# Performance work log

Hardware: AMD Instinct MI355X
Metric: run time of the kernel (lower is better)

Reference implementation:

```python
import jax, jax.numpy as jnp
import numpy as np

N = 2048          # num agents / graph nodes
D = 128           # n_actor == n_map
ALPHA = 0.2       # GAT leakyrelu alpha
NEG = -1e9
X_IDX = [4, 9, 14, 19]   # actors_inter_cat time indices per LSTM step
E_IDX = [0, 4, 9, 14]    # graph_adjs time indices per LSTM step


def setup_inputs() -> dict:
    key = jax.random.key(0)
    ks = jax.random.split(key, 10)
    xavier = lambda k, shape: jax.random.uniform(
        k, shape, jnp.float32, -1.0, 1.0) * 1.414 * np.sqrt(6.0 / (shape[-2] + shape[-1]))
    actors_inter_cat = jax.random.normal(ks[0], (N, 20, D), jnp.float32)
    graph_adjs = jax.random.randint(ks[1], (N, 20, N), 0, 2, jnp.int32)
    # 4 GAT_SRF gates (forget, input, input_cell, output), stacked on leading axis
    Wg = xavier(ks[2], (4, 2 * D, D))          # gate projection W: in=2*D, out=D
    ag = xavier(ks[3], (4, 2 * D))             # attention vector a (2*out_features,)
    W = xavier(ks[4], (D, D))                  # GAT cell output projection
    b = xavier(ks[5], (1, D))
    h0 = xavier(ks[6], (1, D))
    conv_w = jax.random.normal(ks[7], (3, D, D, 2), jnp.float32) * (1.0 / np.sqrt(2 * D))
    conv_b = jax.random.normal(ks[8], (3, D), jnp.float32) * 0.01
    return {"actors_inter_cat": actors_inter_cat, "graph_adjs": graph_adjs,
            "Wg": Wg, "ag": ag, "W": W, "b": b, "h0": h0,
            "conv_w": conv_w, "conv_b": conv_b}


def _gat_gates(gin, mask, Wg, ag):
    # gin: (N, 2D); mask: (N, N) bool. Computes all 4 GAT_SRF gates at once.
    Wh = jnp.einsum('nf,gfo->gno', gin, Wg)                 # (4, N, D)
    s_src = jnp.einsum('gno,go->gn', Wh, ag[:, :D])         # a^T [Wh_i ..]
    s_dst = jnp.einsum('gno,go->gn', Wh, ag[:, D:])
    e = jax.nn.leaky_relu(s_src[:, :, None] + s_dst[:, None, :], ALPHA)  # (4,N,N)
    e = jnp.where(mask[None], e, NEG)
    attn = jax.nn.softmax(e, axis=-1)
    return jax.nn.elu(jnp.einsum('gnm,gmo->gno', attn, Wh))  # concat=True -> ELU


def reference(actors_inter_cat, graph_adjs, Wg, ag, W, b, h0, conv_w, conv_b):
    n = actors_inter_cat.shape[0]
    cell = actors_inter_cat[:, 0, :]
    hidden = jnp.broadcast_to(h0, (n, D))
    outs = []
    for t in range(4):  # fixed 4-step recurrence
        X = actors_inter_cat[:, X_IDX[t], :]
        mask = graph_adjs[:, E_IDX[t], :] > 0
        gin = jnp.concatenate([X, hidden], axis=1)          # (N, 2D)
        g = _gat_gates(gin, mask, Wg, ag)                   # (4, N, D)
        forget = jax.nn.sigmoid(g[0])
        inp_gate = jax.nn.sigmoid(g[1])
        inp_cell = jnp.tanh(g[2])
        out_gate = jax.nn.sigmoid(g[3])
        cell = cell * forget + inp_gate * inp_cell
        hidden = jnp.tanh(cell) * out_gate
        outs.append(jax.nn.sigmoid(hidden @ W + b))
    y = jnp.stack(outs, axis=2)                             # (N, D, 4)
    for l in range(3):  # kernel-2 Conv1d stack: length 4 -> 3 -> 2 -> 1
        y = (jnp.einsum('nct,oc->not', y[:, :, :-1], conv_w[l, :, :, 0])
             + jnp.einsum('nct,oc->not', y[:, :, 1:], conv_w[l, :, :, 1])
             + conv_b[l][None, :, None])
    return y[:, :, 0]                                       # squeeze -> (N, D)
```

## Files before the change

kernel.cpp:

```cpp
#include <hip/hip_runtime.h>

typedef __attribute__((ext_vector_type(8))) short short8;
typedef __attribute__((ext_vector_type(4))) float floatx4;

#define MFMA16(a,b,c) __builtin_amdgcn_mfma_f32_16x16x32_bf16(a,b,c,0,0,0)

__device__ __forceinline__ unsigned short f2bf(float f){
  unsigned u = __float_as_uint(f);
  u += 0x7fffu + ((u >> 16) & 1u);
  return (unsigned short)(u >> 16);
}
__device__ __forceinline__ float sigm(float x){ return 1.f/(1.f+__expf(-x)); }


__global__ __launch_bounds__(256) void prep_kernel(const float* __restrict__ actors,
    const float* __restrict__ Wg, const float* __restrict__ cw, const int* __restrict__ adj,
    float* __restrict__ cell, unsigned short* __restrict__ WgA, float* __restrict__ cwT,
    unsigned long long* __restrict__ bm){
  int bid = blockIdx.x;
  if (bid < 1024){
    int idx = bid*256 + threadIdx.x;
    int n = idx >> 7, c = idx & 127;
    cell[idx] = actors[(size_t)n*2560 + c];
  } else if (bid < 1536){
    int e = (bid-1024)*256 + threadIdx.x;
    int g = e >> 15, o = (e >> 8) & 127, k = e & 255;
    unsigned short v = f2bf(Wg[(size_t)g*32768 + k*128 + o]);
    int off = ((o>>4)*8 + (k>>5))*512 + (((k>>3)&3)*16 + (o&15))*8 + (k&7);
    WgA[(size_t)g*32768 + off] = v;
  } else if (bid < 1728){
    int e = (bid-1536)*256 + threadIdx.x;
    int l = e >> 14, rr = e & 16383, k = rr >> 7, o = rr & 127;
    cwT[(size_t)l*32768 + k*256 + o]       = cw[(size_t)l*32768 + o*256 + k*2];
    cwT[(size_t)l*32768 + k*256 + 128 + o] = cw[(size_t)l*32768 + o*256 + k*2 + 1];
  } else {
    const int E[4] = {0,4,9,14};
    int mb = bid - 1728;
    int t = mb & 3, nblk = mb >> 2;
    int wv = threadIdx.x >> 6, lane = threadIdx.x & 63;
    int n = nblk*4 + wv;
    const int* row = adj + (size_t)n*40960 + (size_t)E[t]*2048;
    unsigned long long* outp = bm + ((size_t)t*2048 + n)*32;
    for (int it=0; it<32; ++it){
      unsigned long long bal = __ballot(row[it*64 + lane] > 0);
      if (lane == 0) outp[it] = bal;
    }
  }
}

__global__ __launch_bounds__(1024) void gatewh_kernel(const float* __restrict__ actors,
    const float* __restrict__ gbuf, float* __restrict__ cell, const float* __restrict__ h0,
    const float* __restrict__ W, const float* __restrict__ bvec,
    const unsigned short* __restrict__ WgA, const float* __restrict__ ag,
    float* __restrict__ y, unsigned short* __restrict__ WhB,
    float* __restrict__ spart, int xoff, int t){
  __shared__ float hl[16][132];
  __shared__ __align__(16) unsigned short ginb[16*264];
  __shared__ float sredS[4][4][16], sredD[4][4][16];
  int bx = blockIdx.x;
  int tile = bx >> 1, ohalf = bx & 1;
  int n0 = tile*16, tid = threadIdx.x;
  int row = tid>>6, q = tid&63;
  {
    int o0 = q*2;
    if (t == 0){
      *(float2*)&hl[row][o0] = *(const float2*)(h0 + o0);
    } else {
      size_t idx = (size_t)(n0+row)*128 + o0;
      float2 ga = *(const float2*)(gbuf+idx);
      float2 gb = *(const float2*)(gbuf+262144+idx);
      float2 gc = *(const float2*)(gbuf+524288+idx);
      float2 gd = *(const float2*)(gbuf+786432+idx);
      float2 cv = *(const float2*)(cell+idx);
      float fg[2]={ga.x,ga.y}, ig[2]={gb.x,gb.y};
      float ic[2]={gc.x,gc.y}, og[2]={gd.x,gd.y};
      float cc[2]={cv.x,cv.y};
      float clv[2];
      #pragma unroll
      for (int j=0;j<2;++j){
        clv[j] = cc[j]*sigm(fg[j]) + sigm(ig[j])*tanhf(ic[j]);
        hl[row][o0+j] = tanhf(clv[j])*sigm(og[j]);
      }
      if (ohalf == 0)
        *(float2*)(cell+idx) = (float2){clv[0],clv[1]};
    }
  }
  __syncthreads();
  if (t >= 1){
    int oc = ohalf*64 + q;
    float a0 = bvec[oc];
    const float* hr = hl[row];
    for (int k=0;k<128;++k)
      a0 += hr[k] * W[(size_t)k*128 + oc];
    y[(size_t)(t-1)*262144 + (size_t)(n0+row)*128 + oc] = sigm(a0);
  }
  if (q < 16){
    const float* ap = actors + (size_t)(n0+row)*2560 + xoff + q*8;
    float4 a = *(const float4*)ap, bb = *(const float4*)(ap+4);
    unsigned short tmp[8] = {f2bf(a.x),f2bf(a.y),f2bf(a.z),f2bf(a.w),
                             f2bf(bb.x),f2bf(bb.y),f2bf(bb.z),f2bf(bb.w)};
    *(uint4*)&ginb[row*264 + q*8] = *(const uint4*)tmp;
  } else if (q < 32){
    int c0 = (q-16)*8;
    unsigned short tmp[8];
    #pragma unroll
    for (int j=0;j<8;++j) tmp[j] = f2bf(hl[row][c0+j]);
    *(uint4*)&ginb[row*264 + 128 + c0] = *(const uint4*)tmp;
  }
  __syncthreads();
  int w = tid>>6, lane = tid&63, quad = lane>>4, l16 = lane&15;
  int m32 = tile>>1, min32 = (tile&1)*16 + l16;
  int qp = min32>>3, jp = min32&7;
  {
    int cidx = w;
    int g = cidx>>2, o16q = cidx&3, o16 = ohalf*4 + o16q;
    floatx4 acc = {0.f,0.f,0.f,0.f};
    const unsigned short* wa = WgA + (size_t)g*32768;
    #pragma unroll
    for (int kh=0; kh<8; ++kh){
      short8 bfr = *(const short8*)&ginb[l16*264 + kh*32 + quad*8];
      short8 a0 = *(const short8*)(wa + (size_t)((o16*8 + kh)*64 + lane)*8);
      acc = MFMA16(a0, bfr, acc);
    }
    float ps = 0.f, pd = 0.f;
    unsigned short* wb = WhB + (size_t)(g*8 + o16)*32768 + m32*512 + qp*128 + jp;
    const float* agp = ag + g*256;
    #pragma unroll
    for (int r=0;r<4;++r){
      int o = o16*16 + quad*4 + r;
      float v = acc[r];
      ps += v*agp[o]; pd += v*agp[128+o];
      wb[(quad*4+r)*8] = f2bf(v);
    }
    ps += __shfl_down(ps,32); ps += __shfl_down(ps,16);
    pd += __shfl_down(pd,32); pd += __shfl_down(pd,16);
    if (lane < 16){ sredS[g][o16q][l16] = ps; sredD[g][o16q][l16] = pd; }
  }
  __syncthreads();
  if (tid < 128){
    int g = tid>>5, which = (tid>>4)&1, n = tid&15;
    float s;
    if (which) s = sredD[g][0][n]+sredD[g][1][n]+sredD[g][2][n]+sredD[g][3][n];
    else       s = sredS[g][0][n]+sredS[g][1][n]+sredS[g][2][n]+sredS[g][3][n];
    spart[(size_t)((ohalf*2 + which)*4 + g)*2048 + n0 + n] = s;
  }
}

__global__ __launch_bounds__(1024) void attn_kernel(const unsigned char* __restrict__ bmb,
    const unsigned short* __restrict__ WhB, const float* __restrict__ spart,
    float* __restrict__ gout, int t){
  __shared__ float obuf[8][32][132];
  __shared__ float zpart[8][32];
  int g = blockIdx.y, n0 = blockIdx.x*32, tid = threadIdx.x;
  int w = tid>>6, lane = tid&63, quad = lane>>4, l16 = lane&15;
  int rh = w>>3, m8 = w&7;
  const float* sS0 = spart + (size_t)(0 + g)*2048;
  const float* sD0 = spart + (size_t)(4 + g)*2048;
  const float* sS1 = spart + (size_t)(8 + g)*2048;
  const float* sD1 = spart + (size_t)(12 + g)*2048;
  int rowg = n0 + rh*16 + l16;
  float srcv = sS0[rowg] + sS1[rowg];
  const unsigned char* mr = bmb + ((size_t)t*2048 + rowg)*256 + m8*32;
  uint4 q0 = *(const uint4*)mr, q1 = *(const uint4*)(mr+16);
  unsigned mwd[8] = {q0.x,q0.y,q0.z,q0.w, q1.x,q1.y,q1.z,q1.w};
  const unsigned short* wb = WhB + (size_t)g*262144;
  float z = 0.f;
  floatx4 acc[8];
  #pragma unroll
  for (int j=0;j<8;++j) acc[j] = (floatx4){0.f,0.f,0.f,0.f};
  #pragma unroll
  for (int c=0; c<8; ++c){
    int mk = m8*256 + c*32 + quad*8;
    float4 sa0 = *(const float4*)(sD0 + mk), sb0 = *(const float4*)(sD0 + mk + 4);
    float4 sa1 = *(const float4*)(sD1 + mk), sb1 = *(const float4*)(sD1 + mk + 4);
    unsigned mb = (mwd[c] >> (quad*8)) & 0xffu;
    float sv[8] = {sa0.x+sa1.x, sa0.y+sa1.y, sa0.z+sa1.z, sa0.w+sa1.w,
                   sb0.x+sb1.x, sb0.y+sb1.y, sb0.z+sb1.z, sb0.w+sb1.w};
    short8 A;
    #pragma unroll
    for (int j=0;j<8;++j){
      float s = srcv + sv[j];
      s = fmaxf(s, 0.2f*s);
      float p = ((mb >> j) & 1u) ? __expf(s) : 0.f;
      z += p;
      A[j] = (short)f2bf(p);
    }
    const unsigned short* bp = wb + (size_t)(m8*8 + c)*512 + lane*8;
    #pragma unroll
    for (int o16=0; o16<8; ++o16){
      short8 bfr = *(const short8*)(bp + (size_t)o16*32768);
      acc[o16] = MFMA16(A, bfr, acc[o16]);
    }
  }
  z += __shfl_down(z,32); z += __shfl_down(z,16);
  if (lane < 16) zpart[m8][rh*16 + l16] = z;
  #pragma unroll
  for (int o16=0;o16<8;++o16)
    #pragma unroll
    for (int r=0;r<4;++r)
      obuf[m8][rh*16 + quad*4 + r][o16*16 + l16] = acc[o16][r];
  __syncthreads();
  {
    int row = tid>>5, c0 = (tid&31)*4;
    float zz = zpart[0][row]+zpart[1][row]+zpart[2][row]+zpart[3][row]
             + zpart[4][row]+zpart[5][row]+zpart[6][row]+zpart[7][row];
    float inv = 1.f / zz;
    float4 res;
    float* rp = &res.x;
    #pragma unroll
    for (int j=0;j<4;++j){
      float v = obuf[0][row][c0+j] + obuf[1][row][c0+j]
              + obuf[2][row][c0+j] + obuf[3][row][c0+j]
              + obuf[4][row][c0+j] + obuf[5][row][c0+j]
              + obuf[6][row][c0+j] + obuf[7][row][c0+j];
      v *= inv;
      rp[j] = v > 0.f ? v : __expf(v) - 1.f;
    }
    *(float4*)(gout + (size_t)g*262144 + (size_t)(n0+row)*128 + c0) = res;
  }
}

__global__ __launch_bounds__(256) void convgate_kernel(const float* __restrict__ gbuf,
    const float* __restrict__ cell, const float* __restrict__ W, const float* __restrict__ bvec,
    const float* __restrict__ y, const float* __restrict__ cwT, const float* __restrict__ cb,
    float* __restrict__ out){
  __shared__ float hl[4][128];
  __shared__ float ylds[4][128][4];
  int tid = threadIdx.x;
  int r = tid >> 6, oc = (tid & 63)*2;
  int n = blockIdx.x*4 + r;
  size_t idx = (size_t)n*128 + oc;
  {
    float2 g0 = *(const float2*)(gbuf+idx),        g1 = *(const float2*)(gbuf+262144+idx);
    float2 g2 = *(const float2*)(gbuf+524288+idx), g3 = *(const float2*)(gbuf+786432+idx);
    float2 cv = *(const float2*)(cell+idx);
    float fg[2]={g0.x,g0.y}, ig[2]={g1.x,g1.y}, ic[2]={g2.x,g2.y}, og[2]={g3.x,g3.y};
    float cc[2]={cv.x,cv.y};
    #pragma unroll
    for (int j=0;j<2;++j){
      float cl = cc[j]*sigm(fg[j]) + sigm(ig[j])*tanhf(ic[j]);
      hl[r][oc+j] = tanhf(cl)*sigm(og[j]);
    }
  }
  {
    float2 y0 = *(const float2*)(y+idx), y1 = *(const float2*)(y+262144+idx),
           y2 = *(const float2*)(y+524288+idx);
    float a0[2]={y0.x,y0.y}, a1[2]={y1.x,y1.y}, a2[2]={y2.x,y2.y};
    #pragma unroll
    for (int j=0;j<2;++j){
      ylds[r][oc+j][0]=a0[j]; ylds[r][oc+j][1]=a1[j]; ylds[r][oc+j][2]=a2[j];
    }
  }
  __syncthreads();
  {
    float2 bb = *(const float2*)(bvec+oc);
    float acc[2] = {bb.x, bb.y};
    const float* hr = hl[r];
    for (int k=0;k<128;++k){
      float hv = hr[k];
      float2 wv = *(const float2*)(W + (size_t)k*128 + oc);
      acc[0]+=hv*wv.x; acc[1]+=hv*wv.y;
    }
    #pragma unroll
    for (int j=0;j<2;++j) ylds[r][oc+j][3] = sigm(acc[j]);
  }
  __syncthreads();
  {
    float a0[2]={0,0}, a1[2]={0,0}, a2[2]={0,0};
    for (int k=0;k<128;++k){
      float2 w0 = *(const float2*)(cwT + k*256 + oc);
      float2 w1 = *(const float2*)(cwT + k*256 + 128 + oc);
      float4 yv = *(const float4*)&ylds[r][k][0];
      float wa[2]={w0.x,w0.y}, wb2[2]={w1.x,w1.y};
      #pragma unroll
      for (int j=0;j<2;++j){
        a0[j] += yv.x*wa[j] + yv.y*wb2[j];
        a1[j] += yv.y*wa[j] + yv.z*wb2[j];
        a2[j] += yv.z*wa[j] + yv.w*wb2[j];
      }
    }
    float2 bb = *(const float2*)(cb+oc);
    float bbv[2]={bb.x,bb.y};
    __syncthreads();
    #pragma unroll
    for (int j=0;j<2;++j){
      ylds[r][oc+j][0]=a0[j]+bbv[j]; ylds[r][oc+j][1]=a1[j]+bbv[j]; ylds[r][oc+j][2]=a2[j]+bbv[j];
    }
    __syncthreads();
  }
  {
    float a0[2]={0,0}, a1[2]={0,0};
    for (int k=0;k<128;++k){
      float2 w0 = *(const float2*)(cwT + 32768 + k*256 + oc);
      float2 w1 = *(const float2*)(cwT + 32768 + k*256 + 128 + oc);
      float4 yv = *(const float4*)&ylds[r][k][0];
      float wa[2]={w0.x,w0.y}, wb2[2]={w1.x,w1.y};
      #pragma unroll
      for (int j=0;j<2;++j){
        a0[j] += yv.x*wa[j] + yv.y*wb2[j];
        a1[j] += yv.y*wa[j] + yv.z*wb2[j];
      }
    }
    float2 bb = *(const float2*)(cb+128+oc);
    float bbv[2]={bb.x,bb.y};
    __syncthreads();
    #pragma unroll
    for (int j=0;j<2;++j){
      ylds[r][oc+j][0]=a0[j]+bbv[j]; ylds[r][oc+j][1]=a1[j]+bbv[j];
    }
    __syncthreads();
  }
  {
    float a0[2]={0,0};
    for (int k=0;k<128;++k){
      float2 w0 = *(const float2*)(cwT + 65536 + k*256 + oc);
      float2 w1 = *(const float2*)(cwT + 65536 + k*256 + 128 + oc);
      float4 yv = *(const float4*)&ylds[r][k][0];
      a0[0] += yv.x*w0.x + yv.y*w1.x;
      a0[1] += yv.x*w0.y + yv.y*w1.y;
    }
    float2 bb = *(const float2*)(cb+256+oc);
    float2 res = {a0[0]+bb.x, a0[1]+bb.y};
    *(float2*)(out+idx) = res;
  }
}

extern "C" void kernel_launch(void* const* d_in, const int* in_sizes, int n_in,
                              void* d_out, int out_size, void* d_ws, size_t ws_size,
                              hipStream_t stream) {
  const float* actors = (const float*)d_in[0];
  const int*   adj    = (const int*)d_in[1];
  const float* Wg     = (const float*)d_in[2];
  const float* ag     = (const float*)d_in[3];
  const float* W      = (const float*)d_in[4];
  const float* b      = (const float*)d_in[5];
  const float* h0     = (const float*)d_in[6];
  const float* cw     = (const float*)d_in[7];
  const float* cb     = (const float*)d_in[8];
  float* out = (float*)d_out;

  char* ws = (char*)d_ws;
  unsigned long long* bm = (unsigned long long*)ws;
  float* cell          = (float*)(ws + (size_t)(2u<<20));
  unsigned short* WgA  = (unsigned short*)(ws + (size_t)(3u<<20));
  float* cwT           = (float*)(ws + (size_t)3407872);
  float* spart         = (float*)(ws + (size_t)3932160);
  unsigned short* WhB  = (unsigned short*)(ws + (size_t)(4u<<20));
  float* gbuf          = (float*)(ws + (size_t)(7u<<20));
  float* yplanes       = (float*)(ws + (size_t)(11u<<20));

  const int XI[4] = {4, 9, 14, 19};

  prep_kernel<<<3776, 256, 0, stream>>>(actors, Wg, cw, adj, cell, WgA, cwT, bm);
  for (int t=0; t<4; ++t){
    gatewh_kernel<<<256, 1024, 0, stream>>>(actors, gbuf, cell, h0, W, b, WgA, ag,
                                            yplanes, WhB, spart, XI[t]*128, t);
    attn_kernel<<<dim3(64,4), 1024, 0, stream>>>((const unsigned char*)bm, WhB,
                                                 spart, gbuf, t);
  }
  convgate_kernel<<<512, 256, 0, stream>>>(gbuf, cell, W, b, yplanes, cwT, cb, out);
}
```

Measured before the change: 617.5 us.

## Fuse attention and next-step gate projection into one pipelined kernel per step

```diff
diff --git a/kernel.cpp b/kernel.cpp
--- a/kernel.cpp
+++ b/kernel.cpp
@@ -48,221 +48,244 @@
   }
 }
 
-__global__ __launch_bounds__(1024) void gatewh_kernel(const float* __restrict__ actors,
-    const float* __restrict__ gbuf, float* __restrict__ cell, const float* __restrict__ h0,
+__global__ __launch_bounds__(512,2) void fused_kernel(const float* __restrict__ actors,
+    float* __restrict__ cell, const float* __restrict__ h0,
     const float* __restrict__ W, const float* __restrict__ bvec,
     const unsigned short* __restrict__ WgA, const float* __restrict__ ag,
-    float* __restrict__ y, unsigned short* __restrict__ WhB,
-    float* __restrict__ spart, int xoff, int t){
+    float* __restrict__ yplanes, const unsigned char* __restrict__ bmb,
+    const unsigned short* __restrict__ whbR, const float* __restrict__ spR,
+    unsigned short* __restrict__ whbW, float* __restrict__ spW,
+    int step, int xoff){
+  __shared__ __align__(16) unsigned char smem[131072];
+  __shared__ __align__(16) unsigned char maskb[4096];
   __shared__ float hl[16][132];
   __shared__ __align__(16) unsigned short ginb[16*264];
-  __shared__ float sredS[4][4][16], sredD[4][4][16];
-  int bx = blockIdx.x;
-  int tile = bx >> 1, ohalf = bx & 1;
-  int n0 = tile*16, tid = threadIdx.x;
-  int row = tid>>6, q = tid&63;
-  {
-    int o0 = q*2;
-    if (t == 0){
-      *(float2*)&hl[row][o0] = *(const float2*)(h0 + o0);
+  __shared__ float sredS[4][8][16], sredD[4][8][16];
+  __shared__ float zpart[4][2][16];
+
+  int bid = blockIdx.x, tid = threadIdx.x;
+  int R0 = bid*16;
+  int w = tid>>6, lane = tid&63, quad = lane>>4, l16 = lane&15;
+  int g = w>>1, mh = w&1;
+
+  if (step >= 0){
+    const unsigned short* wbg = whbR + (size_t)g*262144;
+    const float* sSg = spR + (size_t)g*2048;
+    const float* sDg = spR + (size_t)(4+g)*2048;
+    {
+      const unsigned char* msrc = bmb + ((size_t)step*2048 + R0 + (lane>>3))*256 + mh*128 + (lane&7)*16;
+      unsigned char* mdst = maskb + mh*2048 + lane*16;
+      __builtin_amdgcn_global_load_lds((const void*)msrc, (void*)mdst, 16, 0, 0);
+      __builtin_amdgcn_global_load_lds((const void*)(msrc + 8*256), (void*)(mdst+1024), 16, 0, 0);
+    }
+    float srcv = sSg[R0 + l16];
+    float z = 0.f;
+    floatx4 acc[8];
+    #pragma unroll
+    for (int j=0;j<8;++j) acc[j] = (floatx4){0.f,0.f,0.f,0.f};
+    float4 spA[2], spB[2];
+    {
+      const unsigned short* gsrc = wbg + (size_t)(mh*32)*512 + lane*8;
+      unsigned char* lp = smem + (size_t)(0*8 + w)*8192;
+      #pragma unroll
+      for (int o16=0;o16<8;++o16)
+        __builtin_amdgcn_global_load_lds((const void*)(gsrc + (size_t)o16*32768),
+                                         (void*)(lp + o16*1024), 16, 0, 0);
+      spA[0] = *(const float4*)(sDg + mh*1024 + quad*8);
+      spB[0] = *(const float4*)(sDg + mh*1024 + quad*8 + 4);
+    }
+
+#define SLAB(CC, CUR, NXT) do { \
+    int cc_ = (CC); \
+    if (cc_ < 31){ \
+      const unsigned short* gsrc_ = wbg + (size_t)(mh*32 + cc_ + 1)*512 + lane*8; \
+      unsigned char* lp_ = smem + (size_t)((NXT)*8 + w)*8192; \
+      _Pragma("unroll") \
+      for (int o16=0;o16<8;++o16) \
+        __builtin_amdgcn_global_load_lds((const void*)(gsrc_ + (size_t)o16*32768), \
+                                         (void*)(lp_ + o16*1024), 16, 0, 0); \
+      spA[NXT] = *(const float4*)(sDg + mh*1024 + (cc_+1)*32 + quad*8); \
+      spB[NXT] = *(const float4*)(sDg + mh*1024 + (cc_+1)*32 + quad*8 + 4); \
+      asm volatile("s_waitcnt vmcnt(10)" ::: "memory"); \
+    } else { \
+      asm volatile("s_waitcnt vmcnt(0)" ::: "memory"); \
+    } \
+    __builtin_amdgcn_sched_barrier(0); \
+    unsigned mwd_ = *(const unsigned*)&maskb[mh*2048 + l16*128 + cc_*4]; \
+    unsigned mb_ = (mwd_ >> (quad*8)) & 0xffu; \
+    float4 sa_ = spA[CUR], sb_ = spB[CUR]; \
+    float sv_[8] = {sa_.x,sa_.y,sa_.z,sa_.w, sb_.x,sb_.y,sb_.z,sb_.w}; \
+    short8 A_; \
+    _Pragma("unroll") \
+    for (int j=0;j<8;++j){ \
+      float s_ = srcv + sv_[j]; \
+      s_ = fmaxf(s_, 0.2f*s_); \
+      float p_ = ((mb_ >> j) & 1u) ? __expf(s_) : 0.f; \
+      z += p_; \
+      A_[j] = (short)f2bf(p_); \
+    } \
+    const unsigned char* sb_base_ = smem + (size_t)((CUR)*8 + w)*8192 + lane*16; \
+    _Pragma("unroll") \
+    for (int o16=0; o16<8; ++o16){ \
+      short8 bfr_ = *(const short8*)(sb_base_ + o16*1024); \
+      acc[o16] = MFMA16(A_, bfr_, acc[o16]); \
+    } \
+  } while(0)
+
+    #pragma unroll 1
+    for (int c2=0; c2<16; ++c2){
+      SLAB(2*c2,   0, 1);
+      SLAB(2*c2+1, 1, 0);
+    }
+#undef SLAB
+
+    z += __shfl_down(z,32); z += __shfl_down(z,16);
+    if (lane < 16) zpart[g][mh][l16] = z;
+    __syncthreads();
+    float (*obuf)[16][132] = (float (*)[16][132])smem;
+    if (mh == 0){
+      #pragma unroll
+      for (int o16=0;o16<8;++o16)
+        #pragma unroll
+        for (int r=0;r<4;++r)
+          obuf[g][quad*4+r][o16*16+l16] = acc[o16][r];
+    }
+    __syncthreads();
+    if (mh == 1){
+      #pragma unroll
+      for (int o16=0;o16<8;++o16)
+        #pragma unroll
+        for (int r=0;r<4;++r)
+          obuf[g][quad*4+r][o16*16+l16] += acc[o16][r];
+    }
+    __syncthreads();
+    {
+      int row = tid>>5, o0 = (tid&31)*4;
+      float invz[4];
+      #pragma unroll
+      for (int gg=0;gg<4;++gg) invz[gg] = 1.f / (zpart[gg][0][row] + zpart[gg][1][row]);
+      size_t cidx = (size_t)(R0+row)*128 + o0;
+      float4 cv = *(const float4*)(cell + cidx);
+      float cc4[4] = {cv.x, cv.y, cv.z, cv.w};
+      float clv[4];
+      #pragma unroll
+      for (int j=0;j<4;++j){
+        float gv[4];
+        #pragma unroll
+        for (int gg=0;gg<4;++gg){
+          float v = obuf[gg][row][o0+j] * invz[gg];
+          gv[gg] = v > 0.f ? v : __expf(v) - 1.f;
+        }
+        float cl = cc4[j]*sigm(gv[0]) + sigm(gv[1])*tanhf(gv[2]);
+        clv[j] = cl;
+        hl[row][o0+j] = tanhf(cl)*sigm(gv[3]);
+      }
+      if (step < 3)
+        *(float4*)(cell + cidx) = (float4){clv[0],clv[1],clv[2],clv[3]};
+    }
+    __syncthreads();
+    {
+      int row = tid>>5, oc = (tid&31)*4;
+      float4 bb = *(const float4*)(bvec+oc);
+      float a4[4] = {bb.x, bb.y, bb.z, bb.w};
+      const float* hr = hl[row];
+      #pragma unroll 4
+      for (int k=0;k<128;++k){
+        float hv = hr[k];
+        float4 wv = *(const float4*)(W + (size_t)k*128 + oc);
+        a4[0]+=hv*wv.x; a4[1]+=hv*wv.y; a4[2]+=hv*wv.z; a4[3]+=hv*wv.w;
+      }
+      float* yp = yplanes + (size_t)step*262144 + (size_t)(R0+(tid>>5))*128 + oc;
+      #pragma unroll
+      for (int j=0;j<4;++j) yp[j] = sigm(a4[j]);
+    }
+  } else {
+    int row = tid>>5, o0 = (tid&31)*4;
+    *(float4*)&hl[row][o0] = *(const float4*)(h0 + o0);
+    __syncthreads();
+  }
+
+  if (step >= 3) return;
+
+  {
+    int row = tid>>5, q = tid&31;
+    if (q < 16){
+      const float* ap = actors + (size_t)(R0+row)*2560 + xoff + q*8;
+      float4 a = *(const float4*)ap, bb = *(const float4*)(ap+4);
+      unsigned short tmp[8] = {f2bf(a.x),f2bf(a.y),f2bf(a.z),f2bf(a.w),
+                               f2bf(bb.x),f2bf(bb.y),f2bf(bb.z),f2bf(bb.w)};
+      *(uint4*)&ginb[row*264 + q*8] = *(const uint4*)tmp;
     } else {
-      size_t idx = (size_t)(n0+row)*128 + o0;
-      float2 ga = *(const float2*)(gbuf+idx);
-      float2 gb = *(const float2*)(gbuf+262144+idx);
-      float2 gc = *(const float2*)(gbuf+524288+idx);
-      float2 gd = *(const float2*)(gbuf+786432+idx);
-      float2 cv = *(const float2*)(cell+idx);
-      float fg[2]={ga.x,ga.y}, ig[2]={gb.x,gb.y};
-      float ic[2]={gc.x,gc.y}, og[2]={gd.x,gd.y};
-      float cc[2]={cv.x,cv.y};
-      float clv[2];
-      #pragma unroll
-      for (int j=0;j<2;++j){
-        clv[j] = cc[j]*sigm(fg[j]) + sigm(ig[j])*tanhf(ic[j]);
-        hl[row][o0+j] = tanhf(clv[j])*sigm(og[j]);
-      }
-      if (ohalf == 0)
-        *(float2*)(cell+idx) = (float2){clv[0],clv[1]};
+      int c0 = (q-16)*8;
+      unsigned short tmp[8];
+      #pragma unroll
+      for (int j=0;j<8;++j) tmp[j] = f2bf(hl[row][c0+j]);
+      *(uint4*)&ginb[row*264 + 128 + c0] = *(const uint4*)tmp;
     }
   }
   __syncthreads();
-  if (t >= 1){
-    int oc = ohalf*64 + q;
-    float a0 = bvec[oc];
-    const float* hr = hl[row];
-    for (int k=0;k<128;++k)
-      a0 += hr[k] * W[(size_t)k*128 + oc];
-    y[(size_t)(t-1)*262144 + (size_t)(n0+row)*128 + oc] = sigm(a0);
-  }
-  if (q < 16){
-    const float* ap = actors + (size_t)(n0+row)*2560 + xoff + q*8;
-    float4 a = *(const float4*)ap, bb = *(const float4*)(ap+4);
-    unsigned short tmp[8] = {f2bf(a.x),f2bf(a.y),f2bf(a.z),f2bf(a.w),
-                             f2bf(bb.x),f2bf(bb.y),f2bf(bb.z),f2bf(bb.w)};
-    *(uint4*)&ginb[row*264 + q*8] = *(const uint4*)tmp;
-  } else if (q < 32){
-    int c0 = (q-16)*8;
-    unsigned short tmp[8];
-    #pragma unroll
-    for (int j=0;j<8;++j) tmp[j] = f2bf(hl[row][c0+j]);
-    *(uint4*)&ginb[row*264 + 128 + c0] = *(const uint4*)tmp;
-  }
-  __syncthreads();
-  int w = tid>>6, lane = tid&63, quad = lane>>4, l16 = lane&15;
-  int m32 = tile>>1, min32 = (tile&1)*16 + l16;
-  int qp = min32>>3, jp = min32&7;
-  {
-    int cidx = w;
-    int g = cidx>>2, o16q = cidx&3, o16 = ohalf*4 + o16q;
-    floatx4 acc = {0.f,0.f,0.f,0.f};
-    const unsigned short* wa = WgA + (size_t)g*32768;
-    #pragma unroll
-    for (int kh=0; kh<8; ++kh){
-      short8 bfr = *(const short8*)&ginb[l16*264 + kh*32 + quad*8];
-      short8 a0 = *(const short8*)(wa + (size_t)((o16*8 + kh)*64 + lane)*8);
-      acc = MFMA16(a0, bfr, acc);
-    }
-    float ps = 0.f, pd = 0.f;
-    unsigned short* wb = WhB + (size_t)(g*8 + o16)*32768 + m32*512 + qp*128 + jp;
-    const float* agp = ag + g*256;
-    #pragma unroll
-    for (int r=0;r<4;++r){
-      int o = o16*16 + quad*4 + r;
-      float v = acc[r];
-      ps += v*agp[o]; pd += v*agp[128+o];
-      wb[(quad*4+r)*8] = f2bf(v);
-    }
-    ps += __shfl_down(ps,32); ps += __shfl_down(ps,16);
-    pd += __shfl_down(pd,32); pd += __shfl_down(pd,16);
-    if (lane < 16){ sredS[g][o16q][l16] = ps; sredD[g][o16q][l16] = pd; }
+  {
+    int m32 = bid>>1, min32 = (bid&1)*16 + l16;
+    int qp = min32>>3, jp = min32&7;
+    #pragma unroll
+    for (int ci=0; ci<4; ++ci){
+      int cidx = w*4 + ci;
+      int gg = cidx>>3, o16 = cidx&7;
+      floatx4 acg = {0.f,0.f,0.f,0.f};
+      const unsigned short* wa = WgA + (size_t)gg*32768;
+      #pragma unroll
+      for (int kh=0; kh<8; ++kh){
+        short8 bfr = *(const short8*)&ginb[l16*264 + kh*32 + quad*8];
+        short8 a0 = *(const short8*)(wa + (size_t)((o16*8 + kh)*64 + lane)*8);
+        acg = MFMA16(a0, bfr, acg);
+      }
+      float ps = 0.f, pd = 0.f;
+      unsigned short* wbp = whbW + (size_t)(gg*8 + o16)*32768 + m32*512 + qp*128 + jp;
+      const float* agp = ag + gg*256;
+      #pragma unroll
+      for (int r=0;r<4;++r){
+        int o = o16*16 + quad*4 + r;
+        float v = acg[r];
+        ps += v*agp[o]; pd += v*agp[128+o];
+        wbp[(quad*4+r)*8] = f2bf(v);
+      }
+      ps += __shfl_down(ps,32); ps += __shfl_down(ps,16);
+      pd += __shfl_down(pd,32); pd += __shfl_down(pd,16);
+      if (lane < 16){ sredS[gg][o16][l16] = ps; sredD[gg][o16][l16] = pd; }
+    }
   }
   __syncthreads();
   if (tid < 128){
-    int g = tid>>5, which = (tid>>4)&1, n = tid&15;
-    float s;
-    if (which) s = sredD[g][0][n]+sredD[g][1][n]+sredD[g][2][n]+sredD[g][3][n];
-    else       s = sredS[g][0][n]+sredS[g][1][n]+sredS[g][2][n]+sredS[g][3][n];
-    spart[(size_t)((ohalf*2 + which)*4 + g)*2048 + n0 + n] = s;
-  }
-}
-
-__global__ __launch_bounds__(1024) void attn_kernel(const unsigned char* __restrict__ bmb,
-    const unsigned short* __restrict__ WhB, const float* __restrict__ spart,
-    float* __restrict__ gout, int t){
-  __shared__ float obuf[8][32][132];
-  __shared__ float zpart[8][32];
-  int g = blockIdx.y, n0 = blockIdx.x*32, tid = threadIdx.x;
-  int w = tid>>6, lane = tid&63, quad = lane>>4, l16 = lane&15;
-  int rh = w>>3, m8 = w&7;
-  const float* sS0 = spart + (size_t)(0 + g)*2048;
-  const float* sD0 = spart + (size_t)(4 + g)*2048;
-  const float* sS1 = spart + (size_t)(8 + g)*2048;
-  const float* sD1 = spart + (size_t)(12 + g)*2048;
-  int rowg = n0 + rh*16 + l16;
-  float srcv = sS0[rowg] + sS1[rowg];
-  const unsigned char* mr = bmb + ((size_t)t*2048 + rowg)*256 + m8*32;
-  uint4 q0 = *(const uint4*)mr, q1 = *(const uint4*)(mr+16);
-  unsigned mwd[8] = {q0.x,q0.y,q0.z,q0.w, q1.x,q1.y,q1.z,q1.w};
-  const unsigned short* wb = WhB + (size_t)g*262144;
-  float z = 0.f;
-  floatx4 acc[8];
-  #pragma unroll
-  for (int j=0;j<8;++j) acc[j] = (floatx4){0.f,0.f,0.f,0.f};
-  #pragma unroll
-  for (int c=0; c<8; ++c){
-    int mk = m8*256 + c*32 + quad*8;
-    float4 sa0 = *(const float4*)(sD0 + mk), sb0 = *(const float4*)(sD0 + mk + 4);
-    float4 sa1 = *(const float4*)(sD1 + mk), sb1 = *(const float4*)(sD1 + mk + 4);
-    unsigned mb = (mwd[c] >> (quad*8)) & 0xffu;
-    float sv[8] = {sa0.x+sa1.x, sa0.y+sa1.y, sa0.z+sa1.z, sa0.w+sa1.w,
-                   sb0.x+sb1.x, sb0.y+sb1.y, sb0.z+sb1.z, sb0.w+sb1.w};
-    short8 A;
-    #pragma unroll
-    for (int j=0;j<8;++j){
-      float s = srcv + sv[j];
-      s = fmaxf(s, 0.2f*s);
-      float p = ((mb >> j) & 1u) ? __expf(s) : 0.f;
-      z += p;
-      A[j] = (short)f2bf(p);
-    }
-    const unsigned short* bp = wb + (size_t)(m8*8 + c)*512 + lane*8;
-    #pragma unroll
-    for (int o16=0; o16<8; ++o16){
-      short8 bfr = *(const short8*)(bp + (size_t)o16*32768);
-      acc[o16] = MFMA16(A, bfr, acc[o16]);
-    }
-  }
-  z += __shfl_down(z,32); z += __shfl_down(z,16);
-  if (lane < 16) zpart[m8][rh*16 + l16] = z;
-  #pragma unroll
-  for (int o16=0;o16<8;++o16)
-    #pragma unroll
-    for (int r=0;r<4;++r)
-      obuf[m8][rh*16 + quad*4 + r][o16*16 + l16] = acc[o16][r];
-  __syncthreads();
-  {
-    int row = tid>>5, c0 = (tid&31)*4;
-    float zz = zpart[0][row]+zpart[1][row]+zpart[2][row]+zpart[3][row]
-             + zpart[4][row]+zpart[5][row]+zpart[6][row]+zpart[7][row];
-    float inv = 1.f / zz;
-    float4 res;
-    float* rp = &res.x;
-    #pragma unroll
-    for (int j=0;j<4;++j){
-      float v = obuf[0][row][c0+j] + obuf[1][row][c0+j]
-              + obuf[2][row][c0+j] + obuf[3][row][c0+j]
-              + obuf[4][row][c0+j] + obuf[5][row][c0+j]
-              + obuf[6][row][c0+j] + obuf[7][row][c0+j];
-      v *= inv;
-      rp[j] = v > 0.f ? v : __expf(v) - 1.f;
-    }
-    *(float4*)(gout + (size_t)g*262144 + (size_t)(n0+row)*128 + c0) = res;
-  }
-}
-
-__global__ __launch_bounds__(256) void convgate_kernel(const float* __restrict__ gbuf,
-    const float* __restrict__ cell, const float* __restrict__ W, const float* __restrict__ bvec,
-    const float* __restrict__ y, const float* __restrict__ cwT, const float* __restrict__ cb,
+    int gg = tid>>5, which = (tid>>4)&1, n = tid&15;
+    float s = 0.f;
+    if (which){
+      #pragma unroll
+      for (int o=0;o<8;++o) s += sredD[gg][o][n];
+    } else {
+      #pragma unroll
+      for (int o=0;o<8;++o) s += sredS[gg][o][n];
+    }
+    spW[(size_t)(which*4+gg)*2048 + R0 + n] = s;
+  }
+}
+
+__global__ __launch_bounds__(256) void convgate_kernel(const float* __restrict__ y,
+    const float* __restrict__ cwT, const float* __restrict__ cb,
     float* __restrict__ out){
-  __shared__ float hl[4][128];
   __shared__ float ylds[4][128][4];
   int tid = threadIdx.x;
   int r = tid >> 6, oc = (tid & 63)*2;
   int n = blockIdx.x*4 + r;
   size_t idx = (size_t)n*128 + oc;
   {
-    float2 g0 = *(const float2*)(gbuf+idx),        g1 = *(const float2*)(gbuf+262144+idx);
-    float2 g2 = *(const float2*)(gbuf+524288+idx), g3 = *(const float2*)(gbuf+786432+idx);
-    float2 cv = *(const float2*)(cell+idx);
-    float fg[2]={g0.x,g0.y}, ig[2]={g1.x,g1.y}, ic[2]={g2.x,g2.y}, og[2]={g3.x,g3.y};
-    float cc[2]={cv.x,cv.y};
+    float2 y0 = *(const float2*)(y+idx),        y1 = *(const float2*)(y+262144+idx);
+    float2 y2 = *(const float2*)(y+524288+idx), y3 = *(const float2*)(y+786432+idx);
+    float a0[2]={y0.x,y0.y}, a1[2]={y1.x,y1.y}, a2[2]={y2.x,y2.y}, a3[2]={y3.x,y3.y};
     #pragma unroll
     for (int j=0;j<2;++j){
-      float cl = cc[j]*sigm(fg[j]) + sigm(ig[j])*tanhf(ic[j]);
-      hl[r][oc+j] = tanhf(cl)*sigm(og[j]);
-    }
-  }
-  {
-    float2 y0 = *(const float2*)(y+idx), y1 = *(const float2*)(y+262144+idx),
-           y2 = *(const float2*)(y+524288+idx);
-    float a0[2]={y0.x,y0.y}, a1[2]={y1.x,y1.y}, a2[2]={y2.x,y2.y};
-    #pragma unroll
-    for (int j=0;j<2;++j){
-      ylds[r][oc+j][0]=a0[j]; ylds[r][oc+j][1]=a1[j]; ylds[r][oc+j][2]=a2[j];
-    }
-  }
-  __syncthreads();
-  {
-    float2 bb = *(const float2*)(bvec+oc);
-    float acc[2] = {bb.x, bb.y};
-    const float* hr = hl[r];
-    for (int k=0;k<128;++k){
-      float hv = hr[k];
-      float2 wv = *(const float2*)(W + (size_t)k*128 + oc);
-      acc[0]+=hv*wv.x; acc[1]+=hv*wv.y;
-    }
-    #pragma unroll
-    for (int j=0;j<2;++j) ylds[r][oc+j][3] = sigm(acc[j]);
+      ylds[r][oc+j][0]=a0[j]; ylds[r][oc+j][1]=a1[j];
+      ylds[r][oc+j][2]=a2[j]; ylds[r][oc+j][3]=a3[j];
+    }
   }
   __syncthreads();
   {
@@ -344,19 +367,24 @@
   float* cell          = (float*)(ws + (size_t)(2u<<20));
   unsigned short* WgA  = (unsigned short*)(ws + (size_t)(3u<<20));
   float* cwT           = (float*)(ws + (size_t)3407872);
-  float* spart         = (float*)(ws + (size_t)3932160);
-  unsigned short* WhB  = (unsigned short*)(ws + (size_t)(4u<<20));
-  float* gbuf          = (float*)(ws + (size_t)(7u<<20));
-  float* yplanes       = (float*)(ws + (size_t)(11u<<20));
-
-  const int XI[4] = {4, 9, 14, 19};
+  float* sp0           = (float*)(ws + (size_t)3932160);
+  float* sp1           = (float*)(ws + (size_t)3997696);
+  unsigned short* whb0 = (unsigned short*)(ws + (size_t)(4u<<20));
+  unsigned short* whb1 = (unsigned short*)(ws + (size_t)(6u<<20));
+  float* yplanes       = (float*)(ws + (size_t)(8u<<20));
+
+  const unsigned char* bmb = (const unsigned char*)bm;
 
   prep_kernel<<<3776, 256, 0, stream>>>(actors, Wg, cw, adj, cell, WgA, cwT, bm);
-  for (int t=0; t<4; ++t){
-    gatewh_kernel<<<256, 1024, 0, stream>>>(actors, gbuf, cell, h0, W, b, WgA, ag,
-                                            yplanes, WhB, spart, XI[t]*128, t);
-    attn_kernel<<<dim3(64,4), 1024, 0, stream>>>((const unsigned char*)bm, WhB,
-                                                 spart, gbuf, t);
-  }
-  convgate_kernel<<<512, 256, 0, stream>>>(gbuf, cell, W, b, yplanes, cwT, cb, out);
-}
+  fused_kernel<<<128, 512, 0, stream>>>(actors, cell, h0, W, b, WgA, ag, yplanes,
+                                        bmb, whb0, sp0, whb0, sp0, -1, 4*128);
+  fused_kernel<<<128, 512, 0, stream>>>(actors, cell, h0, W, b, WgA, ag, yplanes,
+                                        bmb, whb0, sp0, whb1, sp1, 0, 9*128);
+  fused_kernel<<<128, 512, 0, stream>>>(actors, cell, h0, W, b, WgA, ag, yplanes,
+                                        bmb, whb1, sp1, whb0, sp0, 1, 14*128);
+  fused_kernel<<<128, 512, 0, stream>>>(actors, cell, h0, W, b, WgA, ag, yplanes,
+                                        bmb, whb0, sp0, whb1, sp1, 2, 19*128);
+  fused_kernel<<<128, 512, 0, stream>>>(actors, cell, h0, W, b, WgA, ag, yplanes,
+                                        bmb, whb1, sp1, whb0, sp0, 3, 0);
+  convgate_kernel<<<512, 256, 0, stream>>>(yplanes, cwT, cb, out);
+}
```

Result: slower. 630.7 us (+2.1%).
